# Kernel tuning notes

Measured on AMD Instinct MI355X. Metric: run time of the kernel, lower is better.

## Reference

```python
import jax, jax.numpy as jnp
import numpy as np

N_NODES = 100000
N_EDGES = 3200000
_EPS = 1e-6

# SE3 layout: [tx, ty, tz, qx, qy, qz, qw] (pypose convention)

def _normalize_se3(T):
    t, q = T[..., :3], T[..., 3:7]
    q = q / jnp.linalg.norm(q, axis=-1, keepdims=True)
    return jnp.concatenate([t, q], axis=-1)

def _qmul(q, r):
    qx, qy, qz, qw = q[..., 0], q[..., 1], q[..., 2], q[..., 3]
    rx, ry, rz, rw = r[..., 0], r[..., 1], r[..., 2], r[..., 3]
    x = qw * rx + qx * rw + qy * rz - qz * ry
    y = qw * ry - qx * rz + qy * rw + qz * rx
    z = qw * rz + qx * ry - qy * rx + qz * rw
    w = qw * rw - qx * rx - qy * ry - qz * rz
    return jnp.stack([x, y, z, w], axis=-1)

def _qrot(q, v):
    # rotate vector v by unit quaternion q: v + 2 w (u x v) + 2 u x (u x v)
    u, w = q[..., :3], q[..., 3:4]
    t = 2.0 * jnp.cross(u, v)
    return v + w * t + jnp.cross(u, t)

def _se3_inv(T):
    t, q = T[..., :3], T[..., 3:7]
    qc = q * jnp.asarray([-1.0, -1.0, -1.0, 1.0], dtype=T.dtype)
    ti = -_qrot(qc, t)
    return jnp.concatenate([ti, qc], axis=-1)

def _se3_mul(A, B):
    ta, qa = A[..., :3], A[..., 3:7]
    tb, qb = B[..., :3], B[..., 3:7]
    return jnp.concatenate([ta + _qrot(qa, tb), _qmul(qa, qb)], axis=-1)

def _so3_log(q):
    # quaternion (xyzw) -> axis-angle 3-vector
    v, w = q[..., :3], q[..., 3]
    n = jnp.linalg.norm(v, axis=-1)
    n_safe = jnp.where(n > _EPS, n, 1.0)
    scale = jnp.where(n > _EPS, 2.0 * jnp.arctan2(n, w) / n_safe, 2.0 / jnp.where(jnp.abs(w) > _EPS, w, 1.0))
    return v * scale[..., None]

def _se3_log(T):
    # SE3 -> se3 = [tau(3), phi(3)], tau = Jl(phi)^{-1} t
    t, q = T[..., :3], T[..., 3:7]
    phi = _so3_log(q)
    theta = jnp.linalg.norm(phi, axis=-1)
    small = theta < _EPS
    th = jnp.where(small, 1.0, theta)
    c = jnp.where(small, 1.0 / 12.0, 1.0 / th**2 - (1.0 + jnp.cos(th)) / (2.0 * th * jnp.sin(th)))
    pxt = jnp.cross(phi, t)
    tau = t - 0.5 * pxt + c[..., None] * jnp.cross(phi, pxt)
    return jnp.concatenate([tau, phi], axis=-1)

def setup_inputs() -> dict:
    key = jax.random.key(0)
    k1, k2, k3 = jax.random.split(key, 3)
    nodes = _normalize_se3(jax.random.normal(k1, (N_NODES, 7), dtype=jnp.float32))
    poses = _normalize_se3(jax.random.normal(k2, (N_EDGES, 7), dtype=jnp.float32))
    edges = jax.random.randint(k3, (N_EDGES, 2), 0, N_NODES, dtype=jnp.int64)
    return {"edges": edges, "poses": poses, "nodes": nodes}

def reference(edges, poses, nodes):
    node1 = nodes[edges[..., 0]]  # [E, 7]
    node2 = nodes[edges[..., 1]]  # [E, 7]
    error = _se3_mul(_se3_mul(_se3_inv(poses), node2), _se3_inv(node1))
    return _se3_log(error)  # [E, 6]
```

## Files before the change

kernel.cpp:

```cpp
#include <hip/hip_runtime.h>
#include <math.h>

#define BLOCK 256
#define EPS 1e-6f

struct F3 { float x, y, z; };
struct F4 { float x, y, z, w; };

__device__ __forceinline__ F3 cross3(F3 a, F3 b) {
    return F3{a.y * b.z - a.z * b.y,
              a.z * b.x - a.x * b.z,
              a.x * b.y - a.y * b.x};
}
__device__ __forceinline__ F3 add3(F3 a, F3 b) { return F3{a.x + b.x, a.y + b.y, a.z + b.z}; }
__device__ __forceinline__ F3 neg3(F3 a) { return F3{-a.x, -a.y, -a.z}; }

__device__ __forceinline__ F3 qrot(F4 q, F3 v) {
    F3 u{q.x, q.y, q.z};
    F3 t = cross3(u, v);
    t.x *= 2.0f; t.y *= 2.0f; t.z *= 2.0f;
    F3 c = cross3(u, t);
    return F3{v.x + q.w * t.x + c.x,
              v.y + q.w * t.y + c.y,
              v.z + q.w * t.z + c.z};
}
__device__ __forceinline__ F4 qmul(F4 q, F4 r) {
    return F4{
        q.w * r.x + q.x * r.w + q.y * r.z - q.z * r.y,
        q.w * r.y - q.x * r.z + q.y * r.w + q.z * r.x,
        q.w * r.z + q.x * r.y - q.y * r.x + q.z * r.w,
        q.w * r.w - q.x * r.x - q.y * r.y - q.z * r.z};
}

__global__ void __launch_bounds__(BLOCK) repack_nodes_kernel(
    const float* __restrict__ nodes, float* __restrict__ nodes8, int total7)
{
    int idx = blockIdx.x * BLOCK + threadIdx.x;
    int stride = gridDim.x * BLOCK;
    for (; idx < total7; idx += stride) {
        int node = idx / 7;
        int comp = idx - node * 7;
        nodes8[node * 8 + comp] = nodes[idx];
    }
}

__device__ __forceinline__ void compute_edge(
    const float* __restrict__ p,
    F3 t1, F4 q1, F3 t2, F4 q2,
    float* __restrict__ o)
{
    F3 tp{p[0], p[1], p[2]};
    F4 qp{p[3], p[4], p[5], p[6]};

    F4 qpc{-qp.x, -qp.y, -qp.z, qp.w};
    F3 tpi = neg3(qrot(qpc, tp));

    F3 tA = add3(tpi, qrot(qpc, t2));
    F4 qA = qmul(qpc, q2);

    F4 q1c{-q1.x, -q1.y, -q1.z, q1.w};
    F3 t1i = neg3(qrot(q1c, t1));

    F3 tE = add3(tA, qrot(qA, t1i));
    F4 qE = qmul(qA, q1c);

    F3 v{qE.x, qE.y, qE.z};
    float w = qE.w;
    float nn = sqrtf(v.x * v.x + v.y * v.y + v.z * v.z);
    float n_safe = (nn > EPS) ? nn : 1.0f;
    float w_safe = (fabsf(w) > EPS) ? w : 1.0f;
    float scale = (nn > EPS) ? (2.0f * atan2f(nn, w) / n_safe)
                             : (2.0f / w_safe);
    F3 phi{v.x * scale, v.y * scale, v.z * scale};

    float theta2 = phi.x * phi.x + phi.y * phi.y + phi.z * phi.z;
    float theta = sqrtf(theta2);
    bool small = theta < EPS;
    float th = small ? 1.0f : theta;
    float s, cth;
    sincosf(th, &s, &cth);
    float c = small ? (1.0f / 12.0f)
                    : (1.0f / (th * th) - (1.0f + cth) / (2.0f * th * s));
    F3 pxt = cross3(phi, tE);
    F3 ppxt = cross3(phi, pxt);
    o[0] = tE.x - 0.5f * pxt.x + c * ppxt.x;
    o[1] = tE.y - 0.5f * pxt.y + c * ppxt.y;
    o[2] = tE.z - 0.5f * pxt.z + c * ppxt.z;
    o[3] = phi.x; o[4] = phi.y; o[5] = phi.z;
}

__global__ void __launch_bounds__(BLOCK) pose_graph_kernel(
    const int* __restrict__ edges,
    const float* __restrict__ poses,
    const float* __restrict__ nodes8,
    float* __restrict__ out,
    int n)
{
    __shared__ float4 sp4[(BLOCK * 7 + 3) / 4];
    __shared__ float  so[BLOCK * 6];

    const int tid = threadIdx.x;
    const long long base = (long long)blockIdx.x * BLOCK;
    const int limit = (int)min((long long)BLOCK, (long long)n - base);
    float* sp = (float*)sp4;

    if (limit == BLOCK) {
        const float4* psrc = (const float4*)(poses + base * 7);
        sp4[tid] = psrc[tid];
        if (tid < (BLOCK * 7 / 4) - BLOCK)
            sp4[tid + BLOCK] = psrc[tid + BLOCK];
    } else {
        const float* psrc = poses + base * 7;
        const int tot = limit * 7;
        for (int idx = tid; idx < tot; idx += BLOCK) sp[idx] = psrc[idx];
    }
    __syncthreads();

    if (tid < limit) {
        const long long e = base + tid;
        const int2 ed = ((const int2*)edges)[e];

        const float4* n1p = (const float4*)(nodes8 + (size_t)ed.x * 8);
        const float4* n2p = (const float4*)(nodes8 + (size_t)ed.y * 8);
        float4 a1 = n1p[0], b1 = n1p[1];
        float4 a2 = n2p[0], b2 = n2p[1];

        F3 t1{a1.x, a1.y, a1.z};
        F4 q1{a1.w, b1.x, b1.y, b1.z};
        F3 t2{a2.x, a2.y, a2.z};
        F4 q2{a2.w, b2.x, b2.y, b2.z};

        compute_edge(&sp[tid * 7], t1, q1, t2, q2, &so[tid * 6]);
    }
    __syncthreads();

    if (limit == BLOCK) {
        float4* odst = (float4*)(out + base * 6);
        float4* sov = (float4*)so;
        odst[tid] = sov[tid];
        if (tid < (BLOCK * 6 / 4) - BLOCK)
            odst[tid + BLOCK] = sov[tid + BLOCK];
    } else {
        float* odst = out + base * 6;
        const int tot = limit * 6;
        for (int idx = tid; idx < tot; idx += BLOCK) odst[idx] = so[idx];
    }
}

__global__ void __launch_bounds__(BLOCK) pose_graph_kernel_fallback(
    const int* __restrict__ edges, const float* __restrict__ poses,
    const float* __restrict__ nodes, float* __restrict__ out, int n)
{
    __shared__ float sp[BLOCK * 7];
    __shared__ float so[BLOCK * 6];
    const int tid = threadIdx.x;
    const long long base = (long long)blockIdx.x * BLOCK;
    const int limit = (int)min((long long)BLOCK, (long long)n - base);
    {
        const float* psrc = poses + base * 7;
        const int tot = limit * 7;
        for (int idx = tid; idx < tot; idx += BLOCK) sp[idx] = psrc[idx];
    }
    __syncthreads();
    if (tid < limit) {
        const long long e = base + tid;
        const int2 ed = ((const int2*)edges)[e];
        const float* n1p = nodes + (size_t)ed.x * 7;
        const float* n2p = nodes + (size_t)ed.y * 7;
        F3 t1{n1p[0], n1p[1], n1p[2]};
        F4 q1{n1p[3], n1p[4], n1p[5], n1p[6]};
        F3 t2{n2p[0], n2p[1], n2p[2]};
        F4 q2{n2p[3], n2p[4], n2p[5], n2p[6]};
        compute_edge(&sp[tid * 7], t1, q1, t2, q2, &so[tid * 6]);
    }
    __syncthreads();
    {
        float* odst = out + base * 6;
        const int tot = limit * 6;
        for (int idx = tid; idx < tot; idx += BLOCK) odst[idx] = so[idx];
    }
}

extern "C" void kernel_launch(void* const* d_in, const int* in_sizes, int n_in,
                              void* d_out, int out_size, void* d_ws, size_t ws_size,
                              hipStream_t stream) {
    const int* edges = (const int*)d_in[0];
    const float* poses = (const float*)d_in[1];
    const float* nodes = (const float*)d_in[2];
    float* out = (float*)d_out;

    const int n_edges = in_sizes[0] / 2;
    const int n_nodes = in_sizes[2] / 7;
    const int grid = (n_edges + BLOCK - 1) / BLOCK;

    const size_t ws_needed = (size_t)n_nodes * 8 * sizeof(float);
    if (ws_size >= ws_needed) {
        float* nodes8 = (float*)d_ws;
        const int total7 = n_nodes * 7;
        const int rgrid = (total7 + BLOCK - 1) / BLOCK;
        repack_nodes_kernel<<<rgrid, BLOCK, 0, stream>>>(nodes, nodes8, total7);
        pose_graph_kernel<<<grid, BLOCK, 0, stream>>>(edges, poses, nodes8, out, n_edges);
    } else {
        pose_graph_kernel_fallback<<<grid, BLOCK, 0, stream>>>(edges, poses, nodes, out, n_edges);
    }
}
```

Measured before the change: 221.9 us.

## Use direct global-to-LDS loads for poses and node gathers, drop block barriers

Poses and gathered node rows are loaded straight into LDS with global_load_lds, using per-wave regions. Node gathers are cooperatively issued with shuffled indices and an XOR swizzle to avoid bank conflicts. Output staging now goes through per-wave LDS, so no __syncthreads is needed. The SE3 log is also simplified algebraically, using the quaternion scalar part to compute the coefficient without sincos. The trade-off is reliance on per-wave waitcnt semantics instead of barriers, and the tail path now uses uncoalesced scalar loads.

New measurement: 209.6 us. -5.6%, faster.

```diff
diff --git a/kernel.cpp b/kernel.cpp
--- a/kernel.cpp
+++ b/kernel.cpp
@@ -3,6 +3,7 @@
 
 #define BLOCK 256
 #define EPS 1e-6f
+
 
 struct F3 { float x, y, z; };
 struct F4 { float x, y, z, w; };
@@ -32,6 +33,53 @@
         q.w * r.w - q.x * r.x - q.y * r.y - q.z * r.z};
 }
 
+__device__ __forceinline__ void se3_error_log(
+    F3 tp, F4 qp, F3 t1, F4 q1, F3 t2, F4 q2, float o[6])
+{
+    F4 qpc{-qp.x, -qp.y, -qp.z, qp.w};
+    F3 tpi = neg3(qrot(qpc, tp));
+
+    F3 tA = add3(tpi, qrot(qpc, t2));
+    F4 qA = qmul(qpc, q2);
+
+    F4 q1c{-q1.x, -q1.y, -q1.z, q1.w};
+    F3 t1i = neg3(qrot(q1c, t1));
+
+    F3 tE = add3(tA, qrot(qA, t1i));
+    F4 qE = qmul(qA, q1c);
+
+    F3 v{qE.x, qE.y, qE.z};
+    float w = qE.w;
+    float nn = sqrtf(v.x * v.x + v.y * v.y + v.z * v.z);
+
+    float scale, c;
+    if (nn > EPS) {
+        float ang = 2.0f * atan2f(nn, w);
+        float rn = 1.0f / nn;
+        float ra = 1.0f / ang;
+        scale = ang * rn;
+        c = ra * ra - 0.5f * w * rn * ra;
+    } else {
+        scale = 2.0f / ((fabsf(w) > EPS) ? w : 1.0f);
+        c = 1.0f / 12.0f;
+    }
+
+    F3 phi{v.x * scale, v.y * scale, v.z * scale};
+    F3 pxt = cross3(phi, tE);
+    F3 ppxt = cross3(phi, pxt);
+    o[0] = tE.x - 0.5f * pxt.x + c * ppxt.x;
+    o[1] = tE.y - 0.5f * pxt.y + c * ppxt.y;
+    o[2] = tE.z - 0.5f * pxt.z + c * ppxt.z;
+    o[3] = phi.x; o[4] = phi.y; o[5] = phi.z;
+}
+
+__device__ __forceinline__ void gload_lds16(const void* g, void* lds) {
+    __builtin_amdgcn_global_load_lds(
+        (const __attribute__((address_space(1))) void*)g,
+        (__attribute__((address_space(3))) void*)lds,
+        16, 0, 0);
+}
+
 __global__ void __launch_bounds__(BLOCK) repack_nodes_kernel(
     const float* __restrict__ nodes, float* __restrict__ nodes8, int total7)
 {
@@ -44,51 +92,6 @@
     }
 }
 
-__device__ __forceinline__ void compute_edge(
-    const float* __restrict__ p,
-    F3 t1, F4 q1, F3 t2, F4 q2,
-    float* __restrict__ o)
-{
-    F3 tp{p[0], p[1], p[2]};
-    F4 qp{p[3], p[4], p[5], p[6]};
-
-    F4 qpc{-qp.x, -qp.y, -qp.z, qp.w};
-    F3 tpi = neg3(qrot(qpc, tp));
-
-    F3 tA = add3(tpi, qrot(qpc, t2));
-    F4 qA = qmul(qpc, q2);
-
-    F4 q1c{-q1.x, -q1.y, -q1.z, q1.w};
-    F3 t1i = neg3(qrot(q1c, t1));
-
-    F3 tE = add3(tA, qrot(qA, t1i));
-    F4 qE = qmul(qA, q1c);
-
-    F3 v{qE.x, qE.y, qE.z};
-    float w = qE.w;
-    float nn = sqrtf(v.x * v.x + v.y * v.y + v.z * v.z);
-    float n_safe = (nn > EPS) ? nn : 1.0f;
-    float w_safe = (fabsf(w) > EPS) ? w : 1.0f;
-    float scale = (nn > EPS) ? (2.0f * atan2f(nn, w) / n_safe)
-                             : (2.0f / w_safe);
-    F3 phi{v.x * scale, v.y * scale, v.z * scale};
-
-    float theta2 = phi.x * phi.x + phi.y * phi.y + phi.z * phi.z;
-    float theta = sqrtf(theta2);
-    bool small = theta < EPS;
-    float th = small ? 1.0f : theta;
-    float s, cth;
-    sincosf(th, &s, &cth);
-    float c = small ? (1.0f / 12.0f)
-                    : (1.0f / (th * th) - (1.0f + cth) / (2.0f * th * s));
-    F3 pxt = cross3(phi, tE);
-    F3 ppxt = cross3(phi, pxt);
-    o[0] = tE.x - 0.5f * pxt.x + c * ppxt.x;
-    o[1] = tE.y - 0.5f * pxt.y + c * ppxt.y;
-    o[2] = tE.z - 0.5f * pxt.z + c * ppxt.z;
-    o[3] = phi.x; o[4] = phi.y; o[5] = phi.z;
-}
-
 __global__ void __launch_bounds__(BLOCK) pose_graph_kernel(
     const int* __restrict__ edges,
     const float* __restrict__ poses,
@@ -96,54 +99,93 @@
     float* __restrict__ out,
     int n)
 {
-    __shared__ float4 sp4[(BLOCK * 7 + 3) / 4];
-    __shared__ float  so[BLOCK * 6];
+    __shared__ float4 SP[448];
+    __shared__ float4 G[4][256];
 
     const int tid = threadIdx.x;
+    const int l = tid & 63;
+    const int w = tid >> 6;
     const long long base = (long long)blockIdx.x * BLOCK;
     const int limit = (int)min((long long)BLOCK, (long long)n - base);
-    float* sp = (float*)sp4;
 
     if (limit == BLOCK) {
-        const float4* psrc = (const float4*)(poses + base * 7);
-        sp4[tid] = psrc[tid];
-        if (tid < (BLOCK * 7 / 4) - BLOCK)
-            sp4[tid + BLOCK] = psrc[tid + BLOCK];
-    } else {
-        const float* psrc = poses + base * 7;
-        const int tot = limit * 7;
-        for (int idx = tid; idx < tot; idx += BLOCK) sp[idx] = psrc[idx];
-    }
-    __syncthreads();
-
-    if (tid < limit) {
         const long long e = base + tid;
         const int2 ed = ((const int2*)edges)[e];
 
-        const float4* n1p = (const float4*)(nodes8 + (size_t)ed.x * 8);
-        const float4* n2p = (const float4*)(nodes8 + (size_t)ed.y * 8);
-        float4 a1 = n1p[0], b1 = n1p[1];
-        float4 a2 = n2p[0], b2 = n2p[1];
+        {
+            const char* psrc = (const char*)poses + base * 28;
+            gload_lds16(psrc + (size_t)(112 * w + l) * 16, &SP[112 * w]);
+            if (l < 48)
+                gload_lds16(psrc + (size_t)(112 * w + 64 + l) * 16, &SP[112 * w + 64]);
+        }
+
+#pragma unroll
+        for (int k = 0; k < 4; ++k) {
+            const int o = k * 16 + (l >> 2);
+            const int m = (l & 3) ^ ((o >> 1) & 3);
+            const int nx = __shfl(ed.x, o, 64);
+            const int ny = __shfl(ed.y, o, 64);
+            const int idx = (m & 2) ? ny : nx;
+            gload_lds16((const char*)nodes8 + ((size_t)idx * 32 + (size_t)(m & 1) * 16),
+                        &G[w][k * 64]);
+        }
+
+        asm volatile("s_waitcnt vmcnt(0)" ::: "memory");
+
+        const float* sp = (const float*)SP;
+        const int p7 = tid * 7;
+        F3 tp{sp[p7 + 0], sp[p7 + 1], sp[p7 + 2]};
+        F4 qp{sp[p7 + 3], sp[p7 + 4], sp[p7 + 5], sp[p7 + 6]};
+
+        const int xo = (l >> 1) & 3;
+        const int b4 = l * 4;
+        float4 a1 = G[w][b4 + (0 ^ xo)];
+        float4 b1 = G[w][b4 + (1 ^ xo)];
+        float4 a2 = G[w][b4 + (2 ^ xo)];
+        float4 b2 = G[w][b4 + (3 ^ xo)];
 
         F3 t1{a1.x, a1.y, a1.z};
         F4 q1{a1.w, b1.x, b1.y, b1.z};
         F3 t2{a2.x, a2.y, a2.z};
         F4 q2{a2.w, b2.x, b2.y, b2.z};
 
-        compute_edge(&sp[tid * 7], t1, q1, t2, q2, &so[tid * 6]);
-    }
-    __syncthreads();
-
-    if (limit == BLOCK) {
+        float o6[6];
+        se3_error_log(tp, qp, t1, q1, t2, q2, o6);
+
+        float* Gf = (float*)&G[w][0];
+        Gf[l * 6 + 0] = o6[0];
+        Gf[l * 6 + 1] = o6[1];
+        Gf[l * 6 + 2] = o6[2];
+        Gf[l * 6 + 3] = o6[3];
+        Gf[l * 6 + 4] = o6[4];
+        Gf[l * 6 + 5] = o6[5];
+        asm volatile("s_waitcnt lgkmcnt(0)" ::: "memory");
+
         float4* odst = (float4*)(out + base * 6);
-        float4* sov = (float4*)so;
-        odst[tid] = sov[tid];
-        if (tid < (BLOCK * 6 / 4) - BLOCK)
-            odst[tid + BLOCK] = sov[tid + BLOCK];
+        odst[w * 96 + l] = G[w][l];
+        if (l < 32)
+            odst[w * 96 + 64 + l] = G[w][64 + l];
     } else {
-        float* odst = out + base * 6;
-        const int tot = limit * 6;
-        for (int idx = tid; idx < tot; idx += BLOCK) odst[idx] = so[idx];
+        if (tid < limit) {
+            const long long e = base + tid;
+            const int2 ed = ((const int2*)edges)[e];
+            const float* pp = poses + e * 7;
+            F3 tp{pp[0], pp[1], pp[2]};
+            F4 qp{pp[3], pp[4], pp[5], pp[6]};
+            const float4* n1p = (const float4*)(nodes8 + (size_t)ed.x * 8);
+            const float4* n2p = (const float4*)(nodes8 + (size_t)ed.y * 8);
+            float4 a1 = n1p[0], b1 = n1p[1];
+            float4 a2 = n2p[0], b2 = n2p[1];
+            F3 t1{a1.x, a1.y, a1.z};
+            F4 q1{a1.w, b1.x, b1.y, b1.z};
+            F3 t2{a2.x, a2.y, a2.z};
+            F4 q2{a2.w, b2.x, b2.y, b2.z};
+            float o6[6];
+            se3_error_log(tp, qp, t1, q1, t2, q2, o6);
+            float* op = out + e * 6;
+            op[0] = o6[0]; op[1] = o6[1]; op[2] = o6[2];
+            op[3] = o6[3]; op[4] = o6[4]; op[5] = o6[5];
+        }
     }
 }
 
@@ -151,33 +193,26 @@
     const int* __restrict__ edges, const float* __restrict__ poses,
     const float* __restrict__ nodes, float* __restrict__ out, int n)
 {
-    __shared__ float sp[BLOCK * 7];
-    __shared__ float so[BLOCK * 6];
     const int tid = threadIdx.x;
     const long long base = (long long)blockIdx.x * BLOCK;
     const int limit = (int)min((long long)BLOCK, (long long)n - base);
-    {
-        const float* psrc = poses + base * 7;
-        const int tot = limit * 7;
-        for (int idx = tid; idx < tot; idx += BLOCK) sp[idx] = psrc[idx];
-    }
-    __syncthreads();
     if (tid < limit) {
         const long long e = base + tid;
         const int2 ed = ((const int2*)edges)[e];
+        const float* pp = poses + e * 7;
+        F3 tp{pp[0], pp[1], pp[2]};
+        F4 qp{pp[3], pp[4], pp[5], pp[6]};
         const float* n1p = nodes + (size_t)ed.x * 7;
         const float* n2p = nodes + (size_t)ed.y * 7;
         F3 t1{n1p[0], n1p[1], n1p[2]};
         F4 q1{n1p[3], n1p[4], n1p[5], n1p[6]};
         F3 t2{n2p[0], n2p[1], n2p[2]};
         F4 q2{n2p[3], n2p[4], n2p[5], n2p[6]};
-        compute_edge(&sp[tid * 7], t1, q1, t2, q2, &so[tid * 6]);
-    }
-    __syncthreads();
-    {
-        float* odst = out + base * 6;
-        const int tot = limit * 6;
-        for (int idx = tid; idx < tot; idx += BLOCK) odst[idx] = so[idx];
+        float o6[6];
+        se3_error_log(tp, qp, t1, q1, t2, q2, o6);
+        float* op = out + e * 6;
+        op[0] = o6[0]; op[1] = o6[1]; op[2] = o6[2];
+        op[3] = o6[3]; op[4] = o6[4]; op[5] = o6[5];
     }
 }
 
```
